# Kernel optimization log

Hardware: AMD Instinct MI355X
Metric: run time of the kernel (lower is better)

## Reference

```python
import jax, jax.numpy as jnp
import numpy as np

STRIDE = (2, 2)
PADDING = (1, 1)
DILATION = (1, 1)
KERNEL = (3, 3)


def _out_hw(h_in, w_in):
    h_out = (h_in + 2 * PADDING[0] - DILATION[0] * (KERNEL[0] - 1) - 1) // STRIDE[0] + 1
    w_out = (w_in + 2 * PADDING[1] - DILATION[1] * (KERNEL[1] - 1) - 1) // STRIDE[1] + 1
    return h_out, w_out


def _stride_permutation(h_out, w_out):
    # Single-shot multiplexing row permutation (mirrors _get_stride_permutation).
    s_h, s_w = STRIDE
    if s_h == 1 and s_w == 1:
        return np.arange(h_out * w_out)
    perm = []
    for si in range(s_h):
        for sj in range(s_w):
            for i in range((h_out + s_h - 1) // s_h):
                ai = i * s_h + si
                if ai >= h_out:
                    continue
                for j in range((w_out + s_w - 1) // s_w):
                    aj = j * s_w + sj
                    if aj >= w_out:
                        continue
                    perm.append(ai * w_out + aj)
    return np.asarray(perm, dtype=np.int32)


def setup_inputs() -> dict:
    key = jax.random.key(0)
    kx, kw, kb = jax.random.split(key, 3)
    x = jax.random.normal(kx, (16, 256, 64, 64), dtype=jnp.float32)
    weight = jax.random.normal(kw, (256, 256, 3, 3), dtype=jnp.float32)
    bias = jax.random.normal(kb, (256,), dtype=jnp.float32)
    return {"x": x, "weight": weight, "bias": bias}


def reference(x, weight, bias):
    # Toeplitz matrix-vector product == grouped strided conv.
    out = jax.lax.conv_general_dilated(
        x, weight,
        window_strides=STRIDE,
        padding=[(PADDING[0], PADDING[0]), (PADDING[1], PADDING[1])],
        rhs_dilation=DILATION,
        dimension_numbers=("NCHW", "OIHW", "NCHW"),
        feature_group_count=1,
    )  # [B, Cout, h_out, w_out]
    b, c, h_out, w_out = out.shape
    perm = jnp.asarray(_stride_permutation(h_out, w_out))
    flat = out.reshape(b, c, h_out * w_out)
    # permuted[new_idx] = flat[perm[new_idx]] (single-shot stride multiplexing)
    permuted = flat[:, :, perm]
    return permuted + bias[None, :, None]
```

## Files before the change

### kernel.cpp

```cpp
#include <hip/hip_runtime.h>
#include <cstdint>

typedef __attribute__((ext_vector_type(8))) __bf16 bf16x8;
typedef __attribute__((ext_vector_type(4))) float f32x4;
typedef __attribute__((ext_vector_type(4))) uint32_t u32x4;

#define NB   16
#define CIN  256
#define COUT 256
#define HP   66
#define WP   66
#define KTOT 2304
#define XPB  (HP*WP*256)
#define XPAD_ELEMS (NB*XPB)

__device__ __forceinline__ uint16_t f2bf(float f) {
  uint32_t u = __builtin_bit_cast(uint32_t, f);
  u = (u + 0x7FFFu + ((u >> 16) & 1u)) >> 16;
  return (uint16_t)u;
}

__global__ void prep_kernel(const float* __restrict__ x, const float* __restrict__ w,
                            uint16_t* __restrict__ xpad, uint16_t* __restrict__ bw) {
  const int bid = blockIdx.x;
  const int tid = threadIdx.x;
  if (bid < 2048) {
    const int lane = tid & 63;
    const int wvi = tid >> 6;
    const int chalf = bid & 1;
    const int h = (bid >> 1) & 63;
    const int b = bid >> 7;
    const int c0 = chalf * 128 + wvi * 32;
    const float* src = x + ((size_t)(b * 256 + c0) * 64 + h) * 64 + lane;
    uint16_t* dst = xpad + ((size_t)(b * HP + h + 1) * WP + lane + 1) * 256 + c0;
    #pragma unroll
    for (int g = 0; g < 4; ++g) {
      u32x4 d;
      #pragma unroll
      for (int k = 0; k < 4; ++k) {
        const float v0 = src[(size_t)(g * 8 + 2 * k + 0) * 4096];
        const float v1 = src[(size_t)(g * 8 + 2 * k + 1) * 4096];
        d[k] = (uint32_t)f2bf(v0) | ((uint32_t)f2bf(v1) << 16);
      }
      *(u32x4*)(dst + g * 8) = d;
    }
  } else if (bid < 3088) {
    const int idx = (bid - 2048) * 256 + tid;
    const int b = idx / 16640;
    const int r = idx - b * 16640;
    uint64_t* base = (uint64_t*)(xpad + (size_t)b * XPB);
    int off;
    if (r < 4224) {
      off = r;
    } else if (r < 8448) {
      off = 274560 + (r - 4224);
    } else if (r < 12544) {
      const int i = r - 8448;
      off = (1 + (i >> 6)) * 4224 + (i & 63);
    } else {
      const int i = r - 12544;
      off = (1 + (i >> 6)) * 4224 + 4160 + (i & 63);
    }
    base[off] = 0;
  } else {
    const int gid = (bid - 3088) * 256 + tid;
    const int co = gid / 288;
    const int r = gid - co * 288;
    const int tap = r >> 5;
    const int ci0 = (r & 31) * 8;
    u32x4 d;
    #pragma unroll
    for (int k = 0; k < 4; ++k) {
      const float v0 = w[((co * 256 + ci0 + 2 * k + 0) * 9) + tap];
      const float v1 = w[((co * 256 + ci0 + 2 * k + 1) * 9) + tap];
      d[k] = (uint32_t)f2bf(v0) | ((uint32_t)f2bf(v1) << 16);
    }
    *(u32x4*)(bw + co * KTOT + tap * 256 + ci0) = d;
  }
}

__device__ __forceinline__ void gl_lds16(const void* g, void* l) {
  __builtin_amdgcn_global_load_lds(
      (__attribute__((address_space(1))) void*)(uintptr_t)g,
      (__attribute__((address_space(3))) void*)(uint32_t)(uintptr_t)l,
      16, 0, 0);
}

__global__ __launch_bounds__(256, 2) void gemm_kernel(
    const uint16_t* __restrict__ xpad, const uint16_t* __restrict__ bw,
    const float* __restrict__ bias, float* __restrict__ out) {
  __shared__ uint16_t lA[2][128 * 64];
  __shared__ uint16_t lB[2][64 * 64];
  const int tid = threadIdx.x;
  const int wv = tid >> 6, lane = tid & 63;
  const int quad = lane >> 4, l15 = lane & 15, l7 = lane & 7;

  const int xcd = blockIdx.x & 7;
  const int grp = blockIdx.x >> 3;
  const int mtile = (xcd << 4) + (grp >> 2);
  const int ntile = grp & 3;
  const int n0 = ntile * 64;
  const int m0 = mtile * 128;
  const int bidx = m0 >> 10;
  const int q0 = m0 & 1023;

  int a_goff[4];
  #pragma unroll
  for (int t = 0; t < 4; ++t) {
    const int slot = t * 256 + tid;
    const int row = slot >> 3;
    const int kc = (slot & 7) ^ (row & 7);
    const int p = q0 + row;
    const int oh = 2 * ((p >> 4) & 15) + ((p >> 9) & 1);
    const int ow = 2 * (p & 15) + ((p >> 8) & 1);
    a_goff[t] = ((bidx * HP + 2 * oh) * WP + 2 * ow) * 256 + kc * 8;
  }
  int b_goff[2];
  #pragma unroll
  for (int t = 0; t < 2; ++t) {
    const int slot = t * 256 + tid;
    const int n = slot >> 3;
    const int kc = (slot & 7) ^ (n & 7);
    b_goff[t] = (n0 + n) * KTOT + kc * 8;
  }

  int aoff[2][2], boff[4][2];
  #pragma unroll
  for (int r = 0; r < 2; ++r)
    #pragma unroll
    for (int s = 0; s < 2; ++s)
      aoff[r][s] = (wv * 32 + r * 16 + l15) * 128 + (((s * 4 + quad) ^ l7) * 16);
  #pragma unroll
  for (int c = 0; c < 4; ++c)
    #pragma unroll
    for (int s = 0; s < 2; ++s)
      boff[c][s] = (c * 16 + l15) * 128 + (((s * 4 + quad) ^ l7) * 16);

  f32x4 acc[2][4];
  #pragma unroll
  for (int r = 0; r < 2; ++r)
    #pragma unroll
    for (int c = 0; c < 4; ++c)
      acc[r][c] = (f32x4){0.f, 0.f, 0.f, 0.f};

  auto stage = [&](int it, int buf) {
    const int tap = it >> 2;
    const int kh = tap / 3, kw = tap - kh * 3;
    const int ci0 = (it & 3) << 6;
    const uint16_t* aptr = xpad + (kh * WP + kw) * 256 + ci0;
    const uint16_t* bptr = bw + tap * 256 + ci0;
    char* la = (char*)&lA[buf][0];
    char* lb = (char*)&lB[buf][0];
    #pragma unroll
    for (int t = 0; t < 4; ++t)
      gl_lds16(aptr + a_goff[t], la + (t * 256 + wv * 64) * 16);
    #pragma unroll
    for (int t = 0; t < 2; ++t)
      gl_lds16(bptr + b_goff[t], lb + (t * 256 + wv * 64) * 16);
  };

  stage(0, 0);
  int buf = 0;
  for (int it = 0; it < 36; ++it) {
    __syncthreads();
    if (it < 35) stage(it + 1, buf ^ 1);
    const char* la = (const char*)&lA[buf][0];
    const char* lb = (const char*)&lB[buf][0];
    #pragma unroll
    for (int s = 0; s < 2; ++s) {
      bf16x8 af[2], bfr[4];
      #pragma unroll
      for (int r = 0; r < 2; ++r) af[r] = *(const bf16x8*)(la + aoff[r][s]);
      #pragma unroll
      for (int c = 0; c < 4; ++c) bfr[c] = *(const bf16x8*)(lb + boff[c][s]);
      #pragma unroll
      for (int r = 0; r < 2; ++r)
        #pragma unroll
        for (int c = 0; c < 4; ++c)
          acc[r][c] = __builtin_amdgcn_mfma_f32_16x16x32_bf16(af[r], bfr[c], acc[r][c], 0, 0, 0);
    }
    buf ^= 1;
  }

  float* obase = out + (size_t)bidx * (COUT * 1024);
  #pragma unroll
  for (int c = 0; c < 4; ++c) {
    const int co = n0 + c * 16 + l15;
    const float bv = bias[co];
    #pragma unroll
    for (int r = 0; r < 2; ++r) {
      const int q = q0 + wv * 32 + r * 16 + quad * 4;
      f32x4 v = acc[r][c];
      v += bv;
      *(f32x4*)(obase + (size_t)co * 1024 + q) = v;
    }
  }
}

extern "C" void kernel_launch(void* const* d_in, const int* in_sizes, int n_in,
                              void* d_out, int out_size, void* d_ws, size_t ws_size,
                              hipStream_t stream) {
  const float* x    = (const float*)d_in[0];
  const float* w    = (const float*)d_in[1];
  const float* bias = (const float*)d_in[2];
  float* out = (float*)d_out;
  uint16_t* xpad = (uint16_t*)d_ws;
  uint16_t* bwq  = xpad + XPAD_ELEMS;

  prep_kernel<<<dim3(3376), dim3(256), 0, stream>>>(x, w, xpad, bwq);
  gemm_kernel<<<dim3(512), dim3(256), 0, stream>>>(xpad, bwq, bias, out);
}
```

Measured before the change: 142.2 us.

## Enlarge GEMM tile to 128x128 with 8 waves and triple-buffered LDS pipeline

The GEMM block now covers a 128x128 output tile with 512 threads arranged as a 4x2 wave grid, halving the grid to 256 blocks. This raises per-block data reuse and halves redundant A-tile loads. LDS staging moves from double to triple buffering, with explicit vmcnt waits so two stages stay in flight while computing. The trade is fewer blocks (256 on a many-CU GPU, one per CU) and higher LDS use, which may reduce latency hiding through occupancy.

New measurement: 143.4 us. About the same (+0.8%).

```diff
diff --git a/kernel.cpp b/kernel.cpp
--- a/kernel.cpp
+++ b/kernel.cpp
@@ -86,28 +86,29 @@
       16, 0, 0);
 }
 
-__global__ __launch_bounds__(256, 2) void gemm_kernel(
+__global__ __launch_bounds__(512, 1) void gemm_kernel(
     const uint16_t* __restrict__ xpad, const uint16_t* __restrict__ bw,
     const float* __restrict__ bias, float* __restrict__ out) {
-  __shared__ uint16_t lA[2][128 * 64];
-  __shared__ uint16_t lB[2][64 * 64];
+  __shared__ uint16_t lA[3][128 * 64];
+  __shared__ uint16_t lB[3][128 * 64];
   const int tid = threadIdx.x;
   const int wv = tid >> 6, lane = tid & 63;
   const int quad = lane >> 4, l15 = lane & 15, l7 = lane & 7;
+  const int wm = wv >> 1, wn = wv & 1;
 
   const int xcd = blockIdx.x & 7;
   const int grp = blockIdx.x >> 3;
-  const int mtile = (xcd << 4) + (grp >> 2);
-  const int ntile = grp & 3;
-  const int n0 = ntile * 64;
+  const int mtile = (xcd << 4) + (grp >> 1);
+  const int ntile = grp & 1;
+  const int n0 = ntile * 128;
   const int m0 = mtile * 128;
   const int bidx = m0 >> 10;
   const int q0 = m0 & 1023;
 
-  int a_goff[4];
-  #pragma unroll
-  for (int t = 0; t < 4; ++t) {
-    const int slot = t * 256 + tid;
+  int a_goff[2];
+  #pragma unroll
+  for (int t = 0; t < 2; ++t) {
+    const int slot = t * 512 + tid;
     const int row = slot >> 3;
     const int kc = (slot & 7) ^ (row & 7);
     const int p = q0 + row;
@@ -118,7 +119,7 @@
   int b_goff[2];
   #pragma unroll
   for (int t = 0; t < 2; ++t) {
-    const int slot = t * 256 + tid;
+    const int slot = t * 512 + tid;
     const int n = slot >> 3;
     const int kc = (slot & 7) ^ (n & 7);
     b_goff[t] = (n0 + n) * KTOT + kc * 8;
@@ -129,12 +130,12 @@
   for (int r = 0; r < 2; ++r)
     #pragma unroll
     for (int s = 0; s < 2; ++s)
-      aoff[r][s] = (wv * 32 + r * 16 + l15) * 128 + (((s * 4 + quad) ^ l7) * 16);
+      aoff[r][s] = (wm * 32 + r * 16 + l15) * 128 + (((s * 4 + quad) ^ l7) * 16);
   #pragma unroll
   for (int c = 0; c < 4; ++c)
     #pragma unroll
     for (int s = 0; s < 2; ++s)
-      boff[c][s] = (c * 16 + l15) * 128 + (((s * 4 + quad) ^ l7) * 16);
+      boff[c][s] = (wn * 64 + c * 16 + l15) * 128 + (((s * 4 + quad) ^ l7) * 16);
 
   f32x4 acc[2][4];
   #pragma unroll
@@ -149,21 +150,17 @@
     const int ci0 = (it & 3) << 6;
     const uint16_t* aptr = xpad + (kh * WP + kw) * 256 + ci0;
     const uint16_t* bptr = bw + tap * 256 + ci0;
-    char* la = (char*)&lA[buf][0];
-    char* lb = (char*)&lB[buf][0];
-    #pragma unroll
-    for (int t = 0; t < 4; ++t)
-      gl_lds16(aptr + a_goff[t], la + (t * 256 + wv * 64) * 16);
+    char* la_ = (char*)&lA[buf][0];
+    char* lb_ = (char*)&lB[buf][0];
     #pragma unroll
     for (int t = 0; t < 2; ++t)
-      gl_lds16(bptr + b_goff[t], lb + (t * 256 + wv * 64) * 16);
+      gl_lds16(aptr + a_goff[t], la_ + (t * 512 + wv * 64) * 16);
+    #pragma unroll
+    for (int t = 0; t < 2; ++t)
+      gl_lds16(bptr + b_goff[t], lb_ + (t * 512 + wv * 64) * 16);
   };
 
-  stage(0, 0);
-  int buf = 0;
-  for (int it = 0; it < 36; ++it) {
-    __syncthreads();
-    if (it < 35) stage(it + 1, buf ^ 1);
+  auto compute = [&](int buf) {
     const char* la = (const char*)&lA[buf][0];
     const char* lb = (const char*)&lB[buf][0];
     #pragma unroll
@@ -179,17 +176,35 @@
         for (int c = 0; c < 4; ++c)
           acc[r][c] = __builtin_amdgcn_mfma_f32_16x16x32_bf16(af[r], bfr[c], acc[r][c], 0, 0, 0);
     }
-    buf ^= 1;
-  }
+  };
+
+  stage(0, 0);
+  stage(1, 1);
+  int bcur = 0;
+  for (int it = 0; it < 35; ++it) {
+    asm volatile("s_waitcnt vmcnt(4)" ::: "memory");
+    __builtin_amdgcn_s_barrier();
+    asm volatile("" ::: "memory");
+    if (it < 34) {
+      int bnext = bcur + 2; if (bnext >= 3) bnext -= 3;
+      stage(it + 2, bnext);
+    }
+    compute(bcur);
+    bcur = (bcur == 2) ? 0 : bcur + 1;
+  }
+  asm volatile("s_waitcnt vmcnt(0)" ::: "memory");
+  __builtin_amdgcn_s_barrier();
+  asm volatile("" ::: "memory");
+  compute(bcur);
 
   float* obase = out + (size_t)bidx * (COUT * 1024);
   #pragma unroll
   for (int c = 0; c < 4; ++c) {
-    const int co = n0 + c * 16 + l15;
+    const int co = n0 + wn * 64 + c * 16 + l15;
     const float bv = bias[co];
     #pragma unroll
     for (int r = 0; r < 2; ++r) {
-      const int q = q0 + wv * 32 + r * 16 + quad * 4;
+      const int q = q0 + wm * 32 + r * 16 + quad * 4;
       f32x4 v = acc[r][c];
       v += bv;
       *(f32x4*)(obase + (size_t)co * 1024 + q) = v;
@@ -208,5 +223,5 @@
   uint16_t* bwq  = xpad + XPAD_ELEMS;
 
   prep_kernel<<<dim3(3376), dim3(256), 0, stream>>>(x, w, xpad, bwq);
-  gemm_kernel<<<dim3(512), dim3(256), 0, stream>>>(xpad, bwq, bias, out);
-}
+  gemm_kernel<<<dim3(256), dim3(512), 0, stream>>>(xpad, bwq, bias, out);
+}
```
